# Kernel optimization log

Measured on AMD Instinct MI355X. Metric: run time of the kernel, lower is better.

Reference implementation:

```python
import jax, jax.numpy as jnp
import numpy as np

B, NPER, K = 32, 256, 32
N, E = B * NPER, B * NPER * 32
H, NF, NG, L = 128, 128, 50, 6
CUTOFF = 10.0
LOG2 = 0.6931471805599453


def _ssp(x):
    # ShiftedSoftplus: softplus(x) - log(2)
    return jax.nn.softplus(x) - LOG2


def setup_inputs() -> dict:
    key = jax.random.key(0)
    ks = jax.random.split(key, 16)
    rng = np.random.default_rng(0)

    pos = jnp.asarray(rng.uniform(0.0, 5.0, size=(N, 3)).astype(np.float32))
    z = jnp.asarray(rng.integers(1, 100, size=(N,)).astype(np.int32))
    batch = jnp.asarray((np.arange(N) // NPER).astype(np.int32))
    # K neighbors per atom, within the same graph, no self-loops; dst sorted
    dst = np.repeat(np.arange(N), K)
    off = rng.integers(1, NPER, size=N * K)
    src = (dst % NPER + off) % NPER + (dst // NPER) * NPER
    edge_index = jnp.asarray(np.stack([src, dst]).astype(np.int32))
    domain_ids = jnp.asarray(rng.integers(0, 5, size=(B,)).astype(np.int32))

    def dense(k, i, o):
        return jax.random.normal(k, (i, o), jnp.float32) / np.sqrt(i)

    def stackw(k, i, o):
        return jax.random.normal(k, (L, i, o), jnp.float32) / np.sqrt(i)

    return {
        'pos': pos, 'z': z, 'batch': batch, 'edge_index': edge_index,
        'domain_ids': domain_ids,
        'embedding': jax.random.normal(ks[0], (100, H), jnp.float32),
        'mlp_w1': stackw(ks[1], NG, NF), 'mlp_b1': jnp.zeros((L, NF), jnp.float32),
        'mlp_w2': stackw(ks[2], NF, NF), 'mlp_b2': jnp.zeros((L, NF), jnp.float32),
        'cf_lin1_w': stackw(ks[3], H, NF),
        'cf_lin2_w': stackw(ks[4], NF, H), 'cf_lin2_b': jnp.zeros((L, H), jnp.float32),
        'int_lin_w': stackw(ks[5], H, H), 'int_lin_b': jnp.zeros((L, H), jnp.float32),
        'out_w1': dense(ks[6], H, H // 2), 'out_b1': jnp.zeros((H // 2,), jnp.float32),
        'out_w2': dense(ks[7], H // 2, 1), 'out_b2': jnp.zeros((1,), jnp.float32),
        'dom_emb': jax.random.normal(ks[8], (5, 64), jnp.float32),
        'film_w1': dense(ks[9], 64, 128), 'film_b1': jnp.zeros((128,), jnp.float32),
        'film_w2': dense(ks[10], 128, 128), 'film_b2': jnp.zeros((128,), jnp.float32),
        'gamma_w': dense(ks[11], 128, H), 'gamma_b': jnp.zeros((H,), jnp.float32),
        'beta_w': dense(ks[12], 128, H), 'beta_b': jnp.zeros((H,), jnp.float32),
    }


def reference(pos, z, batch, edge_index, domain_ids, embedding,
              mlp_w1, mlp_b1, mlp_w2, mlp_b2, cf_lin1_w, cf_lin2_w, cf_lin2_b,
              int_lin_w, int_lin_b, out_w1, out_b1, out_w2, out_b2,
              dom_emb, film_w1, film_b1, film_w2, film_b2,
              gamma_w, gamma_b, beta_w, beta_b):
    n_atoms = pos.shape[0]
    n_graphs = domain_ids.shape[0]
    src, dst = edge_index[0], edge_index[1]

    # edge distances, gaussian smearing, cosine cutoff (computed once)
    d = jnp.sqrt(jnp.sum((pos[src] - pos[dst]) ** 2, axis=-1))          # [E]
    offsets = jnp.linspace(0.0, CUTOFF, NG).astype(pos.dtype)
    coeff = -0.5 / (CUTOFF / (NG - 1)) ** 2
    edge_attr = jnp.exp(coeff * (d[:, None] - offsets) ** 2)            # [E,NG]
    C = 0.5 * (jnp.cos(d * (np.pi / CUTOFF)) + 1.0)                     # [E]

    h = embedding[z]                                                    # [N,H]
    for l in range(L):
        # filter network on gaussian basis, modulated by cosine cutoff
        W = (_ssp(edge_attr @ mlp_w1[l] + mlp_b1[l]) @ mlp_w2[l] + mlp_b2[l]) * C[:, None]  # [E,NF]
        x = h @ cf_lin1_w[l]                                            # [N,NF]
        msg = x[src] * W                                                # [E,NF]
        agg = jax.ops.segment_sum(msg, dst, num_segments=n_atoms)       # [N,NF]
        x = agg @ cf_lin2_w[l] + cf_lin2_b[l]                           # [N,H]
        h = h + _ssp(x) @ int_lin_w[l] + int_lin_b[l]                   # residual

    atom_e = _ssp(h @ out_w1 + out_b1) @ out_w2 + out_b2                # [N,1]
    e_graph = jax.ops.segment_sum(atom_e, batch, num_segments=n_graphs) # [B,1]

    # FiLM domain bias (features are zeros, so gamma path contributes 0 - faithful)
    de = dom_emb[domain_ids]                                            # [B,64]
    film = jax.nn.relu(de @ film_w1 + film_b1) @ film_w2 + film_b2      # [B,128]
    gamma = film @ gamma_w + gamma_b                                    # [B,H]
    beta = film @ beta_w + beta_b                                       # [B,H]
    dummy = jnp.zeros((n_graphs, H), pos.dtype)
    bias = jnp.sum(gamma * dummy + beta, axis=-1)                       # [B]

    # faithful broadcast [B,1]+[B] -> [B,B], then sum(dim=1) as in original
    energy = jnp.sum(e_graph + bias[None, :], axis=1)                   # [B]

    forces = jnp.zeros((n_atoms, 3), energy.dtype)
    stress = jnp.zeros((n_graphs, 3, 3), energy.dtype)
    features = jnp.zeros((n_atoms, H), energy.dtype)
    return energy, forces, stress, features
```

## Files before the change

### kernel.cpp

```cpp
#include <hip/hip_runtime.h>
#include <math.h>

using uint = unsigned int;
typedef _Float16 h2    __attribute__((ext_vector_type(2)));
typedef _Float16 f16x8 __attribute__((ext_vector_type(8)));
typedef float    f32x4 __attribute__((ext_vector_type(4)));

#define N_ATOMS 8192
#define NEDGE   262144
#define KNBR    32
#define NGAUSS  50
#define NLAYER  6
#define NB      32
#define GTAB    1024
#define DMAX    8.6603f
#define FCUT    10.0f
#define MB      1048576

#define LSTRIDE 76
#define S_WT    0
#define S_AS    9728

#define WA_OFF  0
#define WB_OFF  8192
#define AS_OFF  16384
#define TS_OFF  17408
#define LAY_N   18432

#define T_W1    0
#define T_W2    4096
#define T_RBF   12288
#define T_HID   13312
#define TAB_SMEM 15360

#define OW1P_OFF 147456
#define M1_OFF   151552
#define M2_OFF   176128
#define WPACK_N  225280

__device__ __forceinline__ float ssp(float x) {
    return fmaxf(x, 0.0f) + log1pf(expf(-fabsf(x))) - 0.69314718055994531f;
}
__device__ __forceinline__ uint pack2(float a, float b) {
    union { h2 h; uint u; } x;
    h2 v; v.x = (_Float16)a; v.y = (_Float16)b; x.h = v; return x.u;
}
__device__ __forceinline__ h2 u2h(uint u) {
    union { uint u; h2 h; } x; x.u = u; return x.h;
}
__device__ __forceinline__ uint h2u(h2 h) {
    union { h2 h; uint u; } x; x.h = h; return x.u;
}
__device__ __forceinline__ float fdot2f(h2 a, h2 b, float c) {
#if __has_builtin(__builtin_amdgcn_fdot2)
    return __builtin_amdgcn_fdot2(a, b, c, false);
#else
    return fmaf((float)a.y, (float)b.y, fmaf((float)a.x, (float)b.x, c));
#endif
}

__device__ __forceinline__ int swz(int row, int quad) {
    return row * 64 + ((quad ^ (row & 15)) << 2);
}
__device__ __forceinline__ int swzc(int row, int c) {
    return row * 64 + (((c >> 2) ^ (row & 15)) << 2) + (c & 3);
}

__device__ __forceinline__ void stage_sw(uint* dst, const uint* __restrict__ src,
                                         int n16, int tid) {
    for (int i = tid; i < n16; i += 256) {
        uint4 v = ((const uint4*)src)[i];
        *(uint4*)&dst[swz(i >> 4, i & 15)] = v;
    }
}

template<int NCT>
__device__ __forceinline__ void run_gemm_sw(const uint* smA, const uint* smW,
                                            int lane, int nb, f32x4* acc) {
    int m = lane & 15, q = lane >> 4;
    #pragma unroll
    for (int ks = 0; ks < 4; ++ks) {
        int cq = q + ks * 4;
        f16x8 a = *(const f16x8*)&smA[swz(m, cq)];
        #pragma unroll
        for (int ct = 0; ct < NCT; ++ct) {
            int n = nb + ct * 16 + m;
            f16x8 b = *(const f16x8*)&smW[swz(n, cq)];
            acc[ct] = __builtin_amdgcn_mfma_f32_16x16x32_f16(a, b, acc[ct], 0, 0, 0);
        }
    }
}

template<int NCT>
__device__ __forceinline__ void run_gemm(const uint* sm, int as_off, int lane,
                                         int nb, f32x4* acc) {
    int m = lane & 15, q = lane >> 4;
    #pragma unroll
    for (int ks = 0; ks < 4; ++ks) {
        f16x8 a = *(const f16x8*)&sm[as_off + m * LSTRIDE + q * 4 + ks * 16];
        #pragma unroll
        for (int ct = 0; ct < NCT; ++ct) {
            f16x8 b = *(const f16x8*)&sm[S_WT + (nb + ct * 16 + m) * LSTRIDE + q * 4 + ks * 16];
            acc[ct] = __builtin_amdgcn_mfma_f32_16x16x32_f16(a, b, acc[ct], 0, 0, 0);
        }
    }
}

struct SArgs {
    const float *pos; const int *z; const int *ei; const int *dom;
    const float *emb;
    const float *cf1; const float *cf2w; const float *intw; const float *ow1;
    const float *mw1; const float *mw2;
    const float *dome; const float *fw1; const float *fb1;
    const float *fw2; const float *fb2; const float *bw; const float *bb;
    uint2 *epack; float *h; uint *xA;
    float *gbias; uint *wpack; float *out; int out_size;
};

__global__ void __launch_bounds__(256) k_setup(SArgs a) {
    __shared__ __align__(16) uint sm[S_AS + 1216];
    const int tid = threadIdx.x, bid = blockIdx.x;
    const int gidx = bid * 256 + tid, gsz = 512 * 256;
    const int lane = tid & 63, w = tid >> 6;
    const int m = lane & 15, q = lane >> 4;
    const int rowbase = bid * 16;

    for (int i = gidx; i < a.out_size; i += gsz) a.out[i] = 0.0f;

    for (int idx = gidx; idx < WPACK_N; idx += gsz) {
        if (idx < OW1P_OFF) {
            int mat = idx >> 13, e = idx & 8191;
            int kp = e >> 7, cc = e & 127;
            const float* src = (mat < 6) ? (a.cf1 + mat * 16384)
                            : (mat < 12) ? (a.cf2w + (mat - 6) * 16384)
                                         : (a.intw + (mat - 12) * 16384);
            a.wpack[mat * 8192 + cc * 64 + kp] =
                pack2(src[2 * kp * 128 + cc], src[(2 * kp + 1) * 128 + cc]);
        } else if (idx < M1_OFF) {
            int e = idx - OW1P_OFF;
            int kp = e >> 6, cc = e & 63;
            a.wpack[OW1P_OFF + cc * 64 + kp] =
                pack2(a.ow1[2 * kp * 64 + cc], a.ow1[(2 * kp + 1) * 64 + cc]);
        } else if (idx < M2_OFF) {
            int e = idx - M1_OFF;
            int l = e >> 12, r = e & 4095;
            int kp = r >> 7, cc = r & 127;
            int g0 = 2 * kp;
            float va = (g0 < NGAUSS)     ? a.mw1[l*NGAUSS*128 + g0*128 + cc]     : 0.f;
            float vb = (g0 + 1 < NGAUSS) ? a.mw1[l*NGAUSS*128 + (g0+1)*128 + cc] : 0.f;
            a.wpack[idx] = pack2(va, vb);
        } else {
            int e = idx - M2_OFF;
            int l = e >> 13, r = e & 8191;
            int kp = r >> 7, cc = r & 127;
            a.wpack[idx] = pack2(a.mw2[l*16384 + 2*kp*128 + cc],
                                 a.mw2[l*16384 + (2*kp+1)*128 + cc]);
        }
    }

    const float invdelta = (float)(GTAB - 1) / DMAX;
    #pragma unroll
    for (int t = 0; t < 2; ++t) {
        int e = rowbase * KNBR + t * 256 + tid;
        int s = a.ei[e], d = a.ei[NEDGE + e];
        float dx = a.pos[3*s] - a.pos[3*d];
        float dy = a.pos[3*s+1] - a.pos[3*d+1];
        float dz = a.pos[3*s+2] - a.pos[3*d+2];
        float dist = sqrtf(dx*dx + dy*dy + dz*dz);
        float u = dist * invdelta;
        int i0 = (int)u; i0 = (i0 < GTAB - 2) ? i0 : (GTAB - 2);
        float t2 = u - (float)i0;
        uint tb = pack2(t2, 0.0f) & 0xffffu;
        uint2 ep; ep.x = (uint)s; ep.y = (tb << 16) | (uint)i0;
        a.epack[e] = ep;
    }

    for (int i = tid; i < 1024; i += 256) {
        int r = i >> 6, f2 = i & 63;
        int zz = a.z[rowbase + r];
        float2 v = *(const float2*)&a.emb[zz * 128 + f2 * 2];
        *(float2*)&a.h[(rowbase + r) * 128 + f2 * 2] = v;
        sm[S_AS + r * LSTRIDE + f2] = pack2(v.x, v.y);
    }
    for (int i = tid; i < 2048; i += 256) {
        int m4 = i >> 7, cc = i & 127;
        float v[8];
        #pragma unroll
        for (int j = 0; j < 8; ++j) v[j] = a.cf1[(8 * m4 + j) * 128 + cc];
        uint4 pk; pk.x = pack2(v[0], v[1]); pk.y = pack2(v[2], v[3]);
        pk.z = pack2(v[4], v[5]); pk.w = pack2(v[6], v[7]);
        *(uint4*)&sm[cc * LSTRIDE + m4 * 4] = pk;
    }
    __syncthreads();
    {
        f32x4 acc[2] = {{0,0,0,0},{0,0,0,0}};
        run_gemm<2>(sm, S_AS, lane, w * 32, acc);
        #pragma unroll
        for (int ct = 0; ct < 2; ++ct) {
            int n = w * 32 + ct * 16 + m;
            #pragma unroll
            for (int i = 0; i < 4; ++i) {
                float v = acc[ct][i];
                float u = __shfl_xor(v, 1, 64);
                if (!(lane & 1))
                    a.xA[(rowbase + q * 4 + i) * 64 + (n >> 1)] = pack2(v, u);
            }
        }
    }
    __syncthreads();
    if (bid >= 32 && bid < 64) {
        int g = bid - 32;
        float* fs = (float*)sm;
        if (tid < 64) fs[tid] = a.dome[a.dom[g] * 64 + tid];
        __syncthreads();
        if (tid < 128) {
            float acc = a.fb1[tid];
            for (int i = 0; i < 64; ++i) acc = fmaf(fs[i], a.fw1[i*128 + tid], acc);
            fs[64 + tid] = fmaxf(acc, 0.0f);
        }
        __syncthreads();
        if (tid < 128) {
            float acc = a.fb2[tid];
            for (int i = 0; i < 128; ++i) acc = fmaf(fs[64+i], a.fw2[i*128 + tid], acc);
            fs[192 + tid] = acc;
        }
        __syncthreads();
        if (tid < 128) {
            float acc = a.bb[tid];
            for (int i = 0; i < 128; ++i) acc = fmaf(fs[192+i], a.bw[i*128 + tid], acc);
            #pragma unroll
            for (int off = 32; off > 0; off >>= 1) acc += __shfl_down(acc, off, 64);
            if ((tid & 63) == 0) fs[320 + (tid >> 6)] = acc;
        }
        __syncthreads();
        if (tid == 0) a.gbias[g] = fs[320] + fs[321];
    }
}

__global__ void __launch_bounds__(256) k_table(
    const uint* __restrict__ wpack, const float* __restrict__ mb1,
    const float* __restrict__ mb2, uint* __restrict__ tab2) {
    __shared__ __align__(16) uint sm[TAB_SMEM];
    const int tid = threadIdx.x;
    const int l = blockIdx.x >> 5;
    const int base = (blockIdx.x & 31) * 32;
    { const uint4* s4 = (const uint4*)(wpack + M1_OFF + l*4096);
      uint4* d4 = (uint4*)&sm[T_W1];
      for (int i = tid; i < 1024; i += 256) d4[i] = s4[i]; }
    { const uint4* s4 = (const uint4*)(wpack + M2_OFF + l*8192);
      uint4* d4 = (uint4*)&sm[T_W2];
      for (int i = tid; i < 2048; i += 256) d4[i] = s4[i]; }
    const float delta = DMAX / (float)(GTAB - 1);
    const float gstep = FCUT / (float)(NGAUSS - 1);
    const float coeff = -0.5f / (gstep * gstep);
    for (int i = tid; i < 1024; i += 256) {
        int r = i >> 5, kp = i & 31;
        float dv = (float)(base + r) * delta;
        int g0 = 2 * kp;
        float v0 = 0.f, v1 = 0.f;
        if (g0 < NGAUSS)     { float t = dv - (float)g0 * gstep;     v0 = expf(coeff*t*t); }
        if (g0 + 1 < NGAUSS) { float t = dv - (float)(g0+1) * gstep; v1 = expf(coeff*t*t); }
        sm[T_RBF + i] = pack2(v0, v1);
    }
    __syncthreads();
    int tx = tid & 31, ty = tid >> 5, c0 = tx * 4, tr0 = ty * 4;
    float acc[4][4];
    #pragma unroll
    for (int i = 0; i < 4; ++i) { acc[i][0]=0.f; acc[i][1]=0.f; acc[i][2]=0.f; acc[i][3]=0.f; }
    #pragma unroll
    for (int oct = 0; oct < 8; ++oct) {
        int kp0 = oct * 4;
        uint4 w_[4];
        #pragma unroll
        for (int p = 0; p < 4; ++p) w_[p] = *(const uint4*)&sm[T_W1 + (kp0+p)*128 + c0];
        #pragma unroll
        for (int i = 0; i < 4; ++i) {
            uint4 av = *(const uint4*)&sm[T_RBF + (tr0+i)*32 + kp0];
            uint aa[4] = {av.x, av.y, av.z, av.w};
            #pragma unroll
            for (int p = 0; p < 4; ++p) {
                h2 ap = u2h(aa[p]);
                acc[i][0] = fdot2f(ap, u2h(w_[p].x), acc[i][0]);
                acc[i][1] = fdot2f(ap, u2h(w_[p].y), acc[i][1]);
                acc[i][2] = fdot2f(ap, u2h(w_[p].z), acc[i][2]);
                acc[i][3] = fdot2f(ap, u2h(w_[p].w), acc[i][3]);
            }
        }
    }
    float4 b1v = *(const float4*)&mb1[l*128 + c0];
    #pragma unroll
    for (int i = 0; i < 4; ++i) {
        uint2 o;
        o.x = pack2(ssp(acc[i][0] + b1v.x), ssp(acc[i][1] + b1v.y));
        o.y = pack2(ssp(acc[i][2] + b1v.z), ssp(acc[i][3] + b1v.w));
        *(uint2*)&sm[T_HID + (tr0+i)*64 + (c0 >> 1)] = o;
    }
    __syncthreads();
    float acc2[4][4];
    #pragma unroll
    for (int i = 0; i < 4; ++i) { acc2[i][0]=0.f; acc2[i][1]=0.f; acc2[i][2]=0.f; acc2[i][3]=0.f; }
    #pragma unroll 4
    for (int oct = 0; oct < 16; ++oct) {
        int kp0 = oct * 4;
        uint4 w_[4];
        #pragma unroll
        for (int p = 0; p < 4; ++p) w_[p] = *(const uint4*)&sm[T_W2 + (kp0+p)*128 + c0];
        #pragma unroll
        for (int i = 0; i < 4; ++i) {
            uint4 av = *(const uint4*)&sm[T_HID + (tr0+i)*64 + kp0];
            uint aa[4] = {av.x, av.y, av.z, av.w};
            #pragma unroll
            for (int p = 0; p < 4; ++p) {
                h2 ap = u2h(aa[p]);
                acc2[i][0] = fdot2f(ap, u2h(w_[p].x), acc2[i][0]);
                acc2[i][1] = fdot2f(ap, u2h(w_[p].y), acc2[i][1]);
                acc2[i][2] = fdot2f(ap, u2h(w_[p].z), acc2[i][2]);
                acc2[i][3] = fdot2f(ap, u2h(w_[p].w), acc2[i][3]);
            }
        }
    }
    float4 b2v = *(const float4*)&mb2[l*128 + c0];
    #pragma unroll
    for (int i = 0; i < 4; ++i) {
        int row = base + tr0 + i;
        float dv = (float)row * delta;
        float Cd = 0.5f * (cosf(dv * 0.3141592653589793f) + 1.0f);
        uint2 o;
        o.x = pack2((acc2[i][0] + b2v.x)*Cd, (acc2[i][1] + b2v.y)*Cd);
        o.y = pack2((acc2[i][2] + b2v.z)*Cd, (acc2[i][3] + b2v.w)*Cd);
        *(uint2*)&tab2[(l*GTAB + row)*128 + tx*4] = o;
        if (row > 0)
            *(uint2*)&tab2[(l*GTAB + row - 1)*128 + tx*4 + 2] = o;
    }
}

template<bool LAST>
__global__ void __launch_bounds__(256) k_layer(
    float* __restrict__ h, const uint* __restrict__ xin, uint* __restrict__ xout,
    const uint* __restrict__ tab2l, const uint2* __restrict__ epack,
    const uint* __restrict__ w2p, const uint* __restrict__ w3p,
    const uint* __restrict__ w1np,
    const float* __restrict__ b2, const float* __restrict__ b3,
    const float* __restrict__ ob1, const float* __restrict__ ow2,
    const float* __restrict__ ob2, const float* __restrict__ gbias,
    float* __restrict__ out) {
    __shared__ __align__(16) uint sm[LAY_N];
    const int tid = threadIdx.x, bid = blockIdx.x;
    const int lane = tid & 63, w = tid >> 6;
    const int m = lane & 15, q = lane >> 4;
    const int xcd = bid & 7;
    const int j   = bid >> 3;
    const int g   = xcd * 4 + (j >> 4);
    const int sub = j & 15;
    const int rowbase = g * 256 + sub * 16;

    float hr[2][4];
    #pragma unroll
    for (int ct = 0; ct < 2; ++ct)
        #pragma unroll
        for (int i = 0; i < 4; ++i)
            hr[ct][i] = h[(rowbase + q * 4 + i) * 128 + w * 32 + ct * 16 + m];

    stage_sw(&sm[WA_OFF], w2p, 2048, tid);
    {
        const int side = lane >> 5, l5 = lane & 31;
        #pragma unroll
        for (int p = 0; p < 4; ++p) {
            int al = p * 4 + w;
            uint2 ep = epack[(rowbase + al) * KNBR + l5];
            h2 a0; a0.x = (_Float16)0; a0.y = (_Float16)0;
            h2 a1 = a0;
            #pragma unroll 4
            for (int k = 0; k < 16; ++k) {
                int e = 2 * k + side;
                uint s = __shfl(ep.x, e, 64);
                uint y = __shfl(ep.y, e, 64);
                int i0 = (int)(y & 0xffffu);
                uint th = y >> 16;
                h2 t2 = u2h(th | (th << 16));
                uint4 tv = *(const uint4*)&tab2l[i0 * 128 + l5 * 4];
                uint2 xv = *(const uint2*)&xin[s * 64 + l5 * 2];
                h2 w0 = u2h(tv.x) + t2 * (u2h(tv.z) - u2h(tv.x));
                h2 w1 = u2h(tv.y) + t2 * (u2h(tv.w) - u2h(tv.y));
                a0 = a0 + u2h(xv.x) * w0;
                a1 = a1 + u2h(xv.y) * w1;
            }
            uint u0 = h2u(a0), u1 = h2u(a1);
            uint p0 = __shfl_xor(u0, 32, 64), p1 = __shfl_xor(u1, 32, 64);
            if (side == 0) {
                h2 r0 = u2h(u0) + u2h(p0), r1 = u2h(u1) + u2h(p1);
                uint2 o; o.x = h2u(r0); o.y = h2u(r1);
                *(uint2*)&sm[AS_OFF + swzc(al, l5 * 2)] = o;
            }
        }
    }
    __syncthreads();
    stage_sw(&sm[WB_OFF], w3p, 2048, tid);
    {
        f32x4 acc[2] = {{0,0,0,0},{0,0,0,0}};
        run_gemm_sw<2>(&sm[AS_OFF], &sm[WA_OFF], lane, w * 32, acc);
        #pragma unroll
        for (int ct = 0; ct < 2; ++ct) {
            int n = w * 32 + ct * 16 + m;
            float bv = b2[n];
            #pragma unroll
            for (int i = 0; i < 4; ++i) {
                float v = ssp(acc[ct][i] + bv);
                float u = __shfl_xor(v, 1, 64);
                if (!(lane & 1))
                    sm[TS_OFF + swzc(q * 4 + i, n >> 1)] = pack2(v, u);
            }
        }
    }
    __syncthreads();
    stage_sw(&sm[WA_OFF], w1np, LAST ? 1024 : 2048, tid);
    {
        f32x4 acc[2] = {{0,0,0,0},{0,0,0,0}};
        run_gemm_sw<2>(&sm[TS_OFF], &sm[WB_OFF], lane, w * 32, acc);
        #pragma unroll
        for (int ct = 0; ct < 2; ++ct) {
            int n = w * 32 + ct * 16 + m;
            float bv = b3[n];
            #pragma unroll
            for (int i = 0; i < 4; ++i) {
                int r = rowbase + q * 4 + i;
                float hv = hr[ct][i] + acc[ct][i] + bv;
                h[r * 128 + n] = hv;
                float u = __shfl_xor(hv, 1, 64);
                if (!(lane & 1))
                    sm[AS_OFF + swzc(q * 4 + i, n >> 1)] = pack2(hv, u);
            }
        }
    }
    __syncthreads();
    if (!LAST) {
        f32x4 acc[2] = {{0,0,0,0},{0,0,0,0}};
        run_gemm_sw<2>(&sm[AS_OFF], &sm[WA_OFF], lane, w * 32, acc);
        #pragma unroll
        for (int ct = 0; ct < 2; ++ct) {
            int n = w * 32 + ct * 16 + m;
            #pragma unroll
            for (int i = 0; i < 4; ++i) {
                float v = acc[ct][i];
                float u = __shfl_xor(v, 1, 64);
                if (!(lane & 1))
                    xout[(rowbase + q * 4 + i) * 64 + (n >> 1)] = pack2(v, u);
            }
        }
    } else {
        f32x4 acc[1] = {{0,0,0,0}};
        run_gemm_sw<1>(&sm[AS_OFF], &sm[WA_OFF], lane, w * 16, acc);
        int n = w * 16 + m;
        float b1v = ob1[n], w2v = ow2[n];
        float part = 0.f;
        #pragma unroll
        for (int i = 0; i < 4; ++i) part += ssp(acc[0][i] + b1v) * w2v;
        #pragma unroll
        for (int mm = 1; mm < 64; mm <<= 1) part += __shfl_xor(part, mm, 64);
        float* fs = (float*)&sm[TS_OFF];
        if (lane == 0) fs[w] = part;
        __syncthreads();
        if (tid == 0) {
            float bsum = fs[0] + fs[1] + fs[2] + fs[3] + 16.0f * ob2[0];
            float add = 32.0f * bsum;
            if (sub == 0) {
                float sb = 0.f;
                for (int jj = 0; jj < NB; ++jj) sb += gbias[jj];
                add += sb;
            }
            atomicAdd(&out[g], add);
        }
    }
}

extern "C" void kernel_launch(void* const* d_in, const int* in_sizes, int n_in,
                              void* d_out, int out_size, void* d_ws, size_t ws_size,
                              hipStream_t stream) {
    SArgs a;
    a.pos  = (const float*)d_in[0];
    a.z    = (const int*)d_in[1];
    a.ei   = (const int*)d_in[3];
    a.dom  = (const int*)d_in[4];
    a.emb  = (const float*)d_in[5];
    a.mw1  = (const float*)d_in[6];
    const float* mb1 = (const float*)d_in[7];
    a.mw2  = (const float*)d_in[8];
    const float* mb2 = (const float*)d_in[9];
    a.cf1  = (const float*)d_in[10];
    a.cf2w = (const float*)d_in[11];
    const float* cf2b = (const float*)d_in[12];
    a.intw = (const float*)d_in[13];
    const float* intb = (const float*)d_in[14];
    a.ow1  = (const float*)d_in[15];
    const float* ob1  = (const float*)d_in[16];
    const float* ow2  = (const float*)d_in[17];
    const float* ob2  = (const float*)d_in[18];
    a.dome = (const float*)d_in[19];
    a.fw1  = (const float*)d_in[20];
    a.fb1  = (const float*)d_in[21];
    a.fw2  = (const float*)d_in[22];
    a.fb2  = (const float*)d_in[23];
    a.bw   = (const float*)d_in[26];
    a.bb   = (const float*)d_in[27];

    char* ws = (char*)d_ws;
    a.epack   = (uint2*)(ws + 0);
    uint* tab2= (uint*)(ws + 2*MB);
    a.h       = (float*)(ws + 5*MB);
    a.xA      = (uint*)(ws + 9*MB);
    uint* xB  = (uint*)(ws + 11*MB);
    a.gbias   = (float*)(ws + 15*MB);
    a.wpack   = (uint*)(ws + 15*MB + 4096);
    a.out = (float*)d_out;
    a.out_size = out_size;

    k_setup<<<512, 256, 0, stream>>>(a);
    k_table<<<192, 256, 0, stream>>>(a.wpack, mb1, mb2, tab2);

    const uint* xr = a.xA;
    uint* xw = xB;
    for (int l = 0; l < NLAYER; ++l) {
        const uint* w2p = a.wpack + (6 + l) * 8192;
        const uint* w3p = a.wpack + (12 + l) * 8192;
        if (l < NLAYER - 1) {
            k_layer<false><<<512, 256, 0, stream>>>(
                a.h, xr, xw, tab2 + l*GTAB*128, a.epack, w2p, w3p,
                a.wpack + (l + 1) * 8192,
                cf2b + l*128, intb + l*128, ob1, ow2, ob2, a.gbias, a.out);
        } else {
            k_layer<true><<<512, 256, 0, stream>>>(
                a.h, xr, xw, tab2 + l*GTAB*128, a.epack, w2p, w3p,
                a.wpack + OW1P_OFF,
                cf2b + l*128, intb + l*128, ob1, ow2, ob2, a.gbias, a.out);
        }
        const uint* tmp = xr; xr = xw; xw = (uint*)tmp;
    }
}
```

Baseline: 253.5 us.

## Fuse six layer launches into one persistent kernel with per-graph barriers

Merges the table-building kernel into the setup kernel by giving it extra blocks, and replaces the six per-layer launches with one fused kernel. That kernel loops over layers, keeps h in registers, and synchronizes the 16 blocks of each graph through an atomic counter barrier before moving to the next layer. This removes launch overhead and the h round-trip through global memory between layers. It relies on all 16 blocks of a graph being co-resident, and the spin-wait has a timeout that could silently break correctness. Each layer now writes to its own x buffer instead of ping-ponging between two.

```diff
diff --git a/kernel.cpp b/kernel.cpp
--- a/kernel.cpp
+++ b/kernel.cpp
@@ -17,6 +17,10 @@
 #define FCUT    10.0f
 #define MB      1048576
 
+#define NSETUP  512
+#define NTABLE  192
+#define NGRID   (NSETUP + NTABLE)
+
 #define LSTRIDE 76
 #define S_WT    0
 #define S_AS    9728
@@ -34,9 +38,8 @@
 #define TAB_SMEM 15360
 
 #define OW1P_OFF 147456
-#define M1_OFF   151552
-#define M2_OFF   176128
-#define WPACK_N  225280
+#define PACK_END 151552
+#define X_STR    524288
 
 __device__ __forceinline__ float ssp(float x) {
     return fmaxf(x, 0.0f) + log1pf(expf(-fabsf(x))) - 0.69314718055994531f;
@@ -110,24 +113,25 @@
     const float *pos; const int *z; const int *ei; const int *dom;
     const float *emb;
     const float *cf1; const float *cf2w; const float *intw; const float *ow1;
-    const float *mw1; const float *mw2;
+    const float *mw1; const float *mw2; const float *mb1; const float *mb2;
     const float *dome; const float *fw1; const float *fb1;
     const float *fw2; const float *fb2; const float *bw; const float *bb;
     uint2 *epack; float *h; uint *xA;
-    float *gbias; uint *wpack; float *out; int out_size;
+    float *gbias; uint *wpack; uint *tab2; uint *bar;
+    float *out; int out_size;
 };
 
 __global__ void __launch_bounds__(256) k_setup(SArgs a) {
-    __shared__ __align__(16) uint sm[S_AS + 1216];
+    __shared__ __align__(16) uint sm[TAB_SMEM];
     const int tid = threadIdx.x, bid = blockIdx.x;
-    const int gidx = bid * 256 + tid, gsz = 512 * 256;
+    const int gidx = bid * 256 + tid, gsz = NGRID * 256;
     const int lane = tid & 63, w = tid >> 6;
     const int m = lane & 15, q = lane >> 4;
-    const int rowbase = bid * 16;
 
     for (int i = gidx; i < a.out_size; i += gsz) a.out[i] = 0.0f;
-
-    for (int idx = gidx; idx < WPACK_N; idx += gsz) {
+    if (gidx < 256) a.bar[gidx] = 0u;
+
+    for (int idx = gidx; idx < PACK_END; idx += gsz) {
         if (idx < OW1P_OFF) {
             int mat = idx >> 13, e = idx & 8191;
             int kp = e >> 7, cc = e & 127;
@@ -136,214 +140,209 @@
                                          : (a.intw + (mat - 12) * 16384);
             a.wpack[mat * 8192 + cc * 64 + kp] =
                 pack2(src[2 * kp * 128 + cc], src[(2 * kp + 1) * 128 + cc]);
-        } else if (idx < M1_OFF) {
+        } else {
             int e = idx - OW1P_OFF;
             int kp = e >> 6, cc = e & 63;
             a.wpack[OW1P_OFF + cc * 64 + kp] =
                 pack2(a.ow1[2 * kp * 64 + cc], a.ow1[(2 * kp + 1) * 64 + cc]);
-        } else if (idx < M2_OFF) {
-            int e = idx - M1_OFF;
-            int l = e >> 12, r = e & 4095;
-            int kp = r >> 7, cc = r & 127;
-            int g0 = 2 * kp;
+        }
+    }
+
+    if (bid < NSETUP) {
+        const int rowbase = bid * 16;
+        const float invdelta = (float)(GTAB - 1) / DMAX;
+        #pragma unroll
+        for (int t = 0; t < 2; ++t) {
+            int e = rowbase * KNBR + t * 256 + tid;
+            int s = a.ei[e], d = a.ei[NEDGE + e];
+            float dx = a.pos[3*s] - a.pos[3*d];
+            float dy = a.pos[3*s+1] - a.pos[3*d+1];
+            float dz = a.pos[3*s+2] - a.pos[3*d+2];
+            float dist = sqrtf(dx*dx + dy*dy + dz*dz);
+            float u = dist * invdelta;
+            int i0 = (int)u; i0 = (i0 < GTAB - 2) ? i0 : (GTAB - 2);
+            float t2 = u - (float)i0;
+            uint tb = pack2(t2, 0.0f) & 0xffffu;
+            uint2 ep; ep.x = (uint)s; ep.y = (tb << 16) | (uint)i0;
+            a.epack[e] = ep;
+        }
+
+        for (int i = tid; i < 1024; i += 256) {
+            int r = i >> 6, f2 = i & 63;
+            int zz = a.z[rowbase + r];
+            float2 v = *(const float2*)&a.emb[zz * 128 + f2 * 2];
+            *(float2*)&a.h[(rowbase + r) * 128 + f2 * 2] = v;
+            sm[S_AS + r * LSTRIDE + f2] = pack2(v.x, v.y);
+        }
+        for (int i = tid; i < 2048; i += 256) {
+            int m4 = i >> 7, cc = i & 127;
+            float v[8];
+            #pragma unroll
+            for (int j = 0; j < 8; ++j) v[j] = a.cf1[(8 * m4 + j) * 128 + cc];
+            uint4 pk; pk.x = pack2(v[0], v[1]); pk.y = pack2(v[2], v[3]);
+            pk.z = pack2(v[4], v[5]); pk.w = pack2(v[6], v[7]);
+            *(uint4*)&sm[cc * LSTRIDE + m4 * 4] = pk;
+        }
+        __syncthreads();
+        {
+            f32x4 acc[2] = {{0,0,0,0},{0,0,0,0}};
+            run_gemm<2>(sm, S_AS, lane, w * 32, acc);
+            #pragma unroll
+            for (int ct = 0; ct < 2; ++ct) {
+                int n = w * 32 + ct * 16 + m;
+                #pragma unroll
+                for (int i = 0; i < 4; ++i) {
+                    float v = acc[ct][i];
+                    float u = __shfl_xor(v, 1, 64);
+                    if (!(lane & 1))
+                        a.xA[(rowbase + q * 4 + i) * 64 + (n >> 1)] = pack2(v, u);
+                }
+            }
+        }
+        __syncthreads();
+        if (bid >= 32 && bid < 64) {
+            int g = bid - 32;
+            float* fs = (float*)sm;
+            if (tid < 64) fs[tid] = a.dome[a.dom[g] * 64 + tid];
+            __syncthreads();
+            if (tid < 128) {
+                float acc = a.fb1[tid];
+                for (int i = 0; i < 64; ++i) acc = fmaf(fs[i], a.fw1[i*128 + tid], acc);
+                fs[64 + tid] = fmaxf(acc, 0.0f);
+            }
+            __syncthreads();
+            if (tid < 128) {
+                float acc = a.fb2[tid];
+                for (int i = 0; i < 128; ++i) acc = fmaf(fs[64+i], a.fw2[i*128 + tid], acc);
+                fs[192 + tid] = acc;
+            }
+            __syncthreads();
+            if (tid < 128) {
+                float acc = a.bb[tid];
+                for (int i = 0; i < 128; ++i) acc = fmaf(fs[192+i], a.bw[i*128 + tid], acc);
+                #pragma unroll
+                for (int off = 32; off > 0; off >>= 1) acc += __shfl_down(acc, off, 64);
+                if ((tid & 63) == 0) fs[320 + (tid >> 6)] = acc;
+            }
+            __syncthreads();
+            if (tid == 0) a.gbias[g] = fs[320] + fs[321];
+        }
+    } else {
+        const int tb = bid - NSETUP;
+        const int l = tb >> 5;
+        const int base = (tb & 31) * 32;
+        for (int i = tid; i < 4096; i += 256) {
+            int kp = i >> 7, cc = i & 127, g0 = 2 * kp;
             float va = (g0 < NGAUSS)     ? a.mw1[l*NGAUSS*128 + g0*128 + cc]     : 0.f;
             float vb = (g0 + 1 < NGAUSS) ? a.mw1[l*NGAUSS*128 + (g0+1)*128 + cc] : 0.f;
-            a.wpack[idx] = pack2(va, vb);
-        } else {
-            int e = idx - M2_OFF;
-            int l = e >> 13, r = e & 8191;
-            int kp = r >> 7, cc = r & 127;
-            a.wpack[idx] = pack2(a.mw2[l*16384 + 2*kp*128 + cc],
+            sm[T_W1 + i] = pack2(va, vb);
+        }
+        for (int i = tid; i < 8192; i += 256) {
+            int kp = i >> 7, cc = i & 127;
+            sm[T_W2 + i] = pack2(a.mw2[l*16384 + 2*kp*128 + cc],
                                  a.mw2[l*16384 + (2*kp+1)*128 + cc]);
         }
+        const float delta = DMAX / (float)(GTAB - 1);
+        const float gstep = FCUT / (float)(NGAUSS - 1);
+        const float coeff = -0.5f / (gstep * gstep);
+        for (int i = tid; i < 1024; i += 256) {
+            int r = i >> 5, kp = i & 31;
+            float dv = (float)(base + r) * delta;
+            int g0 = 2 * kp;
+            float v0 = 0.f, v1 = 0.f;
+            if (g0 < NGAUSS)     { float t = dv - (float)g0 * gstep;     v0 = expf(coeff*t*t); }
+            if (g0 + 1 < NGAUSS) { float t = dv - (float)(g0+1) * gstep; v1 = expf(coeff*t*t); }
+            sm[T_RBF + i] = pack2(v0, v1);
+        }
+        __syncthreads();
+        int tx = tid & 31, ty = tid >> 5, c0 = tx * 4, tr0 = ty * 4;
+        float acc[4][4];
+        #pragma unroll
+        for (int i = 0; i < 4; ++i) { acc[i][0]=0.f; acc[i][1]=0.f; acc[i][2]=0.f; acc[i][3]=0.f; }
+        #pragma unroll
+        for (int oct = 0; oct < 8; ++oct) {
+            int kp0 = oct * 4;
+            uint4 w_[4];
+            #pragma unroll
+            for (int p = 0; p < 4; ++p) w_[p] = *(const uint4*)&sm[T_W1 + (kp0+p)*128 + c0];
+            #pragma unroll
+            for (int i = 0; i < 4; ++i) {
+                uint4 av = *(const uint4*)&sm[T_RBF + (tr0+i)*32 + kp0];
+                uint aa[4] = {av.x, av.y, av.z, av.w};
+                #pragma unroll
+                for (int p = 0; p < 4; ++p) {
+                    h2 ap = u2h(aa[p]);
+                    acc[i][0] = fdot2f(ap, u2h(w_[p].x), acc[i][0]);
+                    acc[i][1] = fdot2f(ap, u2h(w_[p].y), acc[i][1]);
+                    acc[i][2] = fdot2f(ap, u2h(w_[p].z), acc[i][2]);
+                    acc[i][3] = fdot2f(ap, u2h(w_[p].w), acc[i][3]);
+                }
+            }
+        }
+        float4 b1v = *(const float4*)&a.mb1[l*128 + c0];
+        #pragma unroll
+        for (int i = 0; i < 4; ++i) {
+            uint2 o;
+            o.x = pack2(ssp(acc[i][0] + b1v.x), ssp(acc[i][1] + b1v.y));
+            o.y = pack2(ssp(acc[i][2] + b1v.z), ssp(acc[i][3] + b1v.w));
+            *(uint2*)&sm[T_HID + (tr0+i)*64 + (c0 >> 1)] = o;
+        }
+        __syncthreads();
+        float acc2[4][4];
+        #pragma unroll
+        for (int i = 0; i < 4; ++i) { acc2[i][0]=0.f; acc2[i][1]=0.f; acc2[i][2]=0.f; acc2[i][3]=0.f; }
+        #pragma unroll 4
+        for (int oct = 0; oct < 16; ++oct) {
+            int kp0 = oct * 4;
+            uint4 w_[4];
+            #pragma unroll
+            for (int p = 0; p < 4; ++p) w_[p] = *(const uint4*)&sm[T_W2 + (kp0+p)*128 + c0];
+            #pragma unroll
+            for (int i = 0; i < 4; ++i) {
+                uint4 av = *(const uint4*)&sm[T_HID + (tr0+i)*64 + kp0];
+                uint aa[4] = {av.x, av.y, av.z, av.w};
+                #pragma unroll
+                for (int p = 0; p < 4; ++p) {
+                    h2 ap = u2h(aa[p]);
+                    acc2[i][0] = fdot2f(ap, u2h(w_[p].x), acc2[i][0]);
+                    acc2[i][1] = fdot2f(ap, u2h(w_[p].y), acc2[i][1]);
+                    acc2[i][2] = fdot2f(ap, u2h(w_[p].z), acc2[i][2]);
+                    acc2[i][3] = fdot2f(ap, u2h(w_[p].w), acc2[i][3]);
+                }
+            }
+        }
+        float4 b2v = *(const float4*)&a.mb2[l*128 + c0];
+        #pragma unroll
+        for (int i = 0; i < 4; ++i) {
+            int row = base + tr0 + i;
+            float dv = (float)row * delta;
+            float Cd = 0.5f * (cosf(dv * 0.3141592653589793f) + 1.0f);
+            uint2 o;
+            o.x = pack2((acc2[i][0] + b2v.x)*Cd, (acc2[i][1] + b2v.y)*Cd);
+            o.y = pack2((acc2[i][2] + b2v.z)*Cd, (acc2[i][3] + b2v.w)*Cd);
+            *(uint2*)&a.tab2[(l*GTAB + row)*128 + tx*4] = o;
+            if (row > 0)
+                *(uint2*)&a.tab2[(l*GTAB + row - 1)*128 + tx*4 + 2] = o;
+        }
     }
-
-    const float invdelta = (float)(GTAB - 1) / DMAX;
-    #pragma unroll
-    for (int t = 0; t < 2; ++t) {
-        int e = rowbase * KNBR + t * 256 + tid;
-        int s = a.ei[e], d = a.ei[NEDGE + e];
-        float dx = a.pos[3*s] - a.pos[3*d];
-        float dy = a.pos[3*s+1] - a.pos[3*d+1];
-        float dz = a.pos[3*s+2] - a.pos[3*d+2];
-        float dist = sqrtf(dx*dx + dy*dy + dz*dz);
-        float u = dist * invdelta;
-        int i0 = (int)u; i0 = (i0 < GTAB - 2) ? i0 : (GTAB - 2);
-        float t2 = u - (float)i0;
-        uint tb = pack2(t2, 0.0f) & 0xffffu;
-        uint2 ep; ep.x = (uint)s; ep.y = (tb << 16) | (uint)i0;
-        a.epack[e] = ep;
-    }
-
-    for (int i = tid; i < 1024; i += 256) {
-        int r = i >> 6, f2 = i & 63;
-        int zz = a.z[rowbase + r];
-        float2 v = *(const float2*)&a.emb[zz * 128 + f2 * 2];
-        *(float2*)&a.h[(rowbase + r) * 128 + f2 * 2] = v;
-        sm[S_AS + r * LSTRIDE + f2] = pack2(v.x, v.y);
-    }
-    for (int i = tid; i < 2048; i += 256) {
-        int m4 = i >> 7, cc = i & 127;
-        float v[8];
-        #pragma unroll
-        for (int j = 0; j < 8; ++j) v[j] = a.cf1[(8 * m4 + j) * 128 + cc];
-        uint4 pk; pk.x = pack2(v[0], v[1]); pk.y = pack2(v[2], v[3]);
-        pk.z = pack2(v[4], v[5]); pk.w = pack2(v[6], v[7]);
-        *(uint4*)&sm[cc * LSTRIDE + m4 * 4] = pk;
-    }
-    __syncthreads();
-    {
-        f32x4 acc[2] = {{0,0,0,0},{0,0,0,0}};
-        run_gemm<2>(sm, S_AS, lane, w * 32, acc);
-        #pragma unroll
-        for (int ct = 0; ct < 2; ++ct) {
-            int n = w * 32 + ct * 16 + m;
-            #pragma unroll
-            for (int i = 0; i < 4; ++i) {
-                float v = acc[ct][i];
-                float u = __shfl_xor(v, 1, 64);
-                if (!(lane & 1))
-                    a.xA[(rowbase + q * 4 + i) * 64 + (n >> 1)] = pack2(v, u);
-            }
-        }
-    }
-    __syncthreads();
-    if (bid >= 32 && bid < 64) {
-        int g = bid - 32;
-        float* fs = (float*)sm;
-        if (tid < 64) fs[tid] = a.dome[a.dom[g] * 64 + tid];
-        __syncthreads();
-        if (tid < 128) {
-            float acc = a.fb1[tid];
-            for (int i = 0; i < 64; ++i) acc = fmaf(fs[i], a.fw1[i*128 + tid], acc);
-            fs[64 + tid] = fmaxf(acc, 0.0f);
-        }
-        __syncthreads();
-        if (tid < 128) {
-            float acc = a.fb2[tid];
-            for (int i = 0; i < 128; ++i) acc = fmaf(fs[64+i], a.fw2[i*128 + tid], acc);
-            fs[192 + tid] = acc;
-        }
-        __syncthreads();
-        if (tid < 128) {
-            float acc = a.bb[tid];
-            for (int i = 0; i < 128; ++i) acc = fmaf(fs[192+i], a.bw[i*128 + tid], acc);
-            #pragma unroll
-            for (int off = 32; off > 0; off >>= 1) acc += __shfl_down(acc, off, 64);
-            if ((tid & 63) == 0) fs[320 + (tid >> 6)] = acc;
-        }
-        __syncthreads();
-        if (tid == 0) a.gbias[g] = fs[320] + fs[321];
-    }
-}
-
-__global__ void __launch_bounds__(256) k_table(
-    const uint* __restrict__ wpack, const float* __restrict__ mb1,
-    const float* __restrict__ mb2, uint* __restrict__ tab2) {
-    __shared__ __align__(16) uint sm[TAB_SMEM];
-    const int tid = threadIdx.x;
-    const int l = blockIdx.x >> 5;
-    const int base = (blockIdx.x & 31) * 32;
-    { const uint4* s4 = (const uint4*)(wpack + M1_OFF + l*4096);
-      uint4* d4 = (uint4*)&sm[T_W1];
-      for (int i = tid; i < 1024; i += 256) d4[i] = s4[i]; }
-    { const uint4* s4 = (const uint4*)(wpack + M2_OFF + l*8192);
-      uint4* d4 = (uint4*)&sm[T_W2];
-      for (int i = tid; i < 2048; i += 256) d4[i] = s4[i]; }
-    const float delta = DMAX / (float)(GTAB - 1);
-    const float gstep = FCUT / (float)(NGAUSS - 1);
-    const float coeff = -0.5f / (gstep * gstep);
-    for (int i = tid; i < 1024; i += 256) {
-        int r = i >> 5, kp = i & 31;
-        float dv = (float)(base + r) * delta;
-        int g0 = 2 * kp;
-        float v0 = 0.f, v1 = 0.f;
-        if (g0 < NGAUSS)     { float t = dv - (float)g0 * gstep;     v0 = expf(coeff*t*t); }
-        if (g0 + 1 < NGAUSS) { float t = dv - (float)(g0+1) * gstep; v1 = expf(coeff*t*t); }
-        sm[T_RBF + i] = pack2(v0, v1);
-    }
-    __syncthreads();
-    int tx = tid & 31, ty = tid >> 5, c0 = tx * 4, tr0 = ty * 4;
-    float acc[4][4];
-    #pragma unroll
-    for (int i = 0; i < 4; ++i) { acc[i][0]=0.f; acc[i][1]=0.f; acc[i][2]=0.f; acc[i][3]=0.f; }
-    #pragma unroll
-    for (int oct = 0; oct < 8; ++oct) {
-        int kp0 = oct * 4;
-        uint4 w_[4];
-        #pragma unroll
-        for (int p = 0; p < 4; ++p) w_[p] = *(const uint4*)&sm[T_W1 + (kp0+p)*128 + c0];
-        #pragma unroll
-        for (int i = 0; i < 4; ++i) {
-            uint4 av = *(const uint4*)&sm[T_RBF + (tr0+i)*32 + kp0];
-            uint aa[4] = {av.x, av.y, av.z, av.w};
-            #pragma unroll
-            for (int p = 0; p < 4; ++p) {
-                h2 ap = u2h(aa[p]);
-                acc[i][0] = fdot2f(ap, u2h(w_[p].x), acc[i][0]);
-                acc[i][1] = fdot2f(ap, u2h(w_[p].y), acc[i][1]);
-                acc[i][2] = fdot2f(ap, u2h(w_[p].z), acc[i][2]);
-                acc[i][3] = fdot2f(ap, u2h(w_[p].w), acc[i][3]);
-            }
-        }
-    }
-    float4 b1v = *(const float4*)&mb1[l*128 + c0];
-    #pragma unroll
-    for (int i = 0; i < 4; ++i) {
-        uint2 o;
-        o.x = pack2(ssp(acc[i][0] + b1v.x), ssp(acc[i][1] + b1v.y));
-        o.y = pack2(ssp(acc[i][2] + b1v.z), ssp(acc[i][3] + b1v.w));
-        *(uint2*)&sm[T_HID + (tr0+i)*64 + (c0 >> 1)] = o;
-    }
-    __syncthreads();
-    float acc2[4][4];
-    #pragma unroll
-    for (int i = 0; i < 4; ++i) { acc2[i][0]=0.f; acc2[i][1]=0.f; acc2[i][2]=0.f; acc2[i][3]=0.f; }
-    #pragma unroll 4
-    for (int oct = 0; oct < 16; ++oct) {
-        int kp0 = oct * 4;
-        uint4 w_[4];
-        #pragma unroll
-        for (int p = 0; p < 4; ++p) w_[p] = *(const uint4*)&sm[T_W2 + (kp0+p)*128 + c0];
-        #pragma unroll
-        for (int i = 0; i < 4; ++i) {
-            uint4 av = *(const uint4*)&sm[T_HID + (tr0+i)*64 + kp0];
-            uint aa[4] = {av.x, av.y, av.z, av.w};
-            #pragma unroll
-            for (int p = 0; p < 4; ++p) {
-                h2 ap = u2h(aa[p]);
-                acc2[i][0] = fdot2f(ap, u2h(w_[p].x), acc2[i][0]);
-                acc2[i][1] = fdot2f(ap, u2h(w_[p].y), acc2[i][1]);
-                acc2[i][2] = fdot2f(ap, u2h(w_[p].z), acc2[i][2]);
-                acc2[i][3] = fdot2f(ap, u2h(w_[p].w), acc2[i][3]);
-            }
-        }
-    }
-    float4 b2v = *(const float4*)&mb2[l*128 + c0];
-    #pragma unroll
-    for (int i = 0; i < 4; ++i) {
-        int row = base + tr0 + i;
-        float dv = (float)row * delta;
-        float Cd = 0.5f * (cosf(dv * 0.3141592653589793f) + 1.0f);
-        uint2 o;
-        o.x = pack2((acc2[i][0] + b2v.x)*Cd, (acc2[i][1] + b2v.y)*Cd);
-        o.y = pack2((acc2[i][2] + b2v.z)*Cd, (acc2[i][3] + b2v.w)*Cd);
-        *(uint2*)&tab2[(l*GTAB + row)*128 + tx*4] = o;
-        if (row > 0)
-            *(uint2*)&tab2[(l*GTAB + row - 1)*128 + tx*4 + 2] = o;
-    }
-}
-
-template<bool LAST>
-__global__ void __launch_bounds__(256) k_layer(
-    float* __restrict__ h, const uint* __restrict__ xin, uint* __restrict__ xout,
-    const uint* __restrict__ tab2l, const uint2* __restrict__ epack,
-    const uint* __restrict__ w2p, const uint* __restrict__ w3p,
-    const uint* __restrict__ w1np,
-    const float* __restrict__ b2, const float* __restrict__ b3,
-    const float* __restrict__ ob1, const float* __restrict__ ow2,
-    const float* __restrict__ ob2, const float* __restrict__ gbias,
-    float* __restrict__ out) {
+}
+
+struct LArgs {
+    const float* h;
+    const uint* x0;
+    uint* xb;
+    const uint* tab2;
+    const uint2* epack;
+    const uint* wpack;
+    const float* cf2b;
+    const float* intb;
+    const float* ob1; const float* ow2; const float* ob2;
+    const float* gbias;
+    float* out;
+    uint* bar;
+};
+
+__global__ void __launch_bounds__(256, 2) k_fused(LArgs a) {
     __shared__ __align__(16) uint sm[LAY_N];
     const int tid = threadIdx.x, bid = blockIdx.x;
     const int lane = tid & 63, w = tid >> 6;
@@ -359,116 +358,141 @@
     for (int ct = 0; ct < 2; ++ct)
         #pragma unroll
         for (int i = 0; i < 4; ++i)
-            hr[ct][i] = h[(rowbase + q * 4 + i) * 128 + w * 32 + ct * 16 + m];
-
-    stage_sw(&sm[WA_OFF], w2p, 2048, tid);
-    {
-        const int side = lane >> 5, l5 = lane & 31;
-        #pragma unroll
-        for (int p = 0; p < 4; ++p) {
-            int al = p * 4 + w;
-            uint2 ep = epack[(rowbase + al) * KNBR + l5];
-            h2 a0; a0.x = (_Float16)0; a0.y = (_Float16)0;
-            h2 a1 = a0;
-            #pragma unroll 4
-            for (int k = 0; k < 16; ++k) {
-                int e = 2 * k + side;
-                uint s = __shfl(ep.x, e, 64);
-                uint y = __shfl(ep.y, e, 64);
-                int i0 = (int)(y & 0xffffu);
-                uint th = y >> 16;
-                h2 t2 = u2h(th | (th << 16));
-                uint4 tv = *(const uint4*)&tab2l[i0 * 128 + l5 * 4];
-                uint2 xv = *(const uint2*)&xin[s * 64 + l5 * 2];
-                h2 w0 = u2h(tv.x) + t2 * (u2h(tv.z) - u2h(tv.x));
-                h2 w1 = u2h(tv.y) + t2 * (u2h(tv.w) - u2h(tv.y));
-                a0 = a0 + u2h(xv.x) * w0;
-                a1 = a1 + u2h(xv.y) * w1;
-            }
-            uint u0 = h2u(a0), u1 = h2u(a1);
-            uint p0 = __shfl_xor(u0, 32, 64), p1 = __shfl_xor(u1, 32, 64);
-            if (side == 0) {
-                h2 r0 = u2h(u0) + u2h(p0), r1 = u2h(u1) + u2h(p1);
-                uint2 o; o.x = h2u(r0); o.y = h2u(r1);
-                *(uint2*)&sm[AS_OFF + swzc(al, l5 * 2)] = o;
-            }
-        }
-    }
-    __syncthreads();
-    stage_sw(&sm[WB_OFF], w3p, 2048, tid);
-    {
-        f32x4 acc[2] = {{0,0,0,0},{0,0,0,0}};
-        run_gemm_sw<2>(&sm[AS_OFF], &sm[WA_OFF], lane, w * 32, acc);
-        #pragma unroll
-        for (int ct = 0; ct < 2; ++ct) {
-            int n = w * 32 + ct * 16 + m;
-            float bv = b2[n];
-            #pragma unroll
-            for (int i = 0; i < 4; ++i) {
-                float v = ssp(acc[ct][i] + bv);
-                float u = __shfl_xor(v, 1, 64);
-                if (!(lane & 1))
-                    sm[TS_OFF + swzc(q * 4 + i, n >> 1)] = pack2(v, u);
-            }
-        }
-    }
-    __syncthreads();
-    stage_sw(&sm[WA_OFF], w1np, LAST ? 1024 : 2048, tid);
-    {
-        f32x4 acc[2] = {{0,0,0,0},{0,0,0,0}};
-        run_gemm_sw<2>(&sm[TS_OFF], &sm[WB_OFF], lane, w * 32, acc);
-        #pragma unroll
-        for (int ct = 0; ct < 2; ++ct) {
-            int n = w * 32 + ct * 16 + m;
-            float bv = b3[n];
-            #pragma unroll
-            for (int i = 0; i < 4; ++i) {
-                int r = rowbase + q * 4 + i;
-                float hv = hr[ct][i] + acc[ct][i] + bv;
-                h[r * 128 + n] = hv;
-                float u = __shfl_xor(hv, 1, 64);
-                if (!(lane & 1))
-                    sm[AS_OFF + swzc(q * 4 + i, n >> 1)] = pack2(hv, u);
-            }
-        }
-    }
-    __syncthreads();
-    if (!LAST) {
-        f32x4 acc[2] = {{0,0,0,0},{0,0,0,0}};
-        run_gemm_sw<2>(&sm[AS_OFF], &sm[WA_OFF], lane, w * 32, acc);
-        #pragma unroll
-        for (int ct = 0; ct < 2; ++ct) {
-            int n = w * 32 + ct * 16 + m;
-            #pragma unroll
-            for (int i = 0; i < 4; ++i) {
-                float v = acc[ct][i];
-                float u = __shfl_xor(v, 1, 64);
-                if (!(lane & 1))
-                    xout[(rowbase + q * 4 + i) * 64 + (n >> 1)] = pack2(v, u);
-            }
-        }
-    } else {
-        f32x4 acc[1] = {{0,0,0,0}};
-        run_gemm_sw<1>(&sm[AS_OFF], &sm[WA_OFF], lane, w * 16, acc);
-        int n = w * 16 + m;
-        float b1v = ob1[n], w2v = ow2[n];
-        float part = 0.f;
-        #pragma unroll
-        for (int i = 0; i < 4; ++i) part += ssp(acc[0][i] + b1v) * w2v;
-        #pragma unroll
-        for (int mm = 1; mm < 64; mm <<= 1) part += __shfl_xor(part, mm, 64);
-        float* fs = (float*)&sm[TS_OFF];
-        if (lane == 0) fs[w] = part;
-        __syncthreads();
-        if (tid == 0) {
-            float bsum = fs[0] + fs[1] + fs[2] + fs[3] + 16.0f * ob2[0];
-            float add = 32.0f * bsum;
-            if (sub == 0) {
-                float sb = 0.f;
-                for (int jj = 0; jj < NB; ++jj) sb += gbias[jj];
-                add += sb;
-            }
-            atomicAdd(&out[g], add);
+            hr[ct][i] = a.h[(rowbase + q * 4 + i) * 128 + w * 32 + ct * 16 + m];
+
+    const uint* xr = a.x0;
+    uint* xw = a.xb;
+
+    #pragma unroll 1
+    for (int l = 0; l < NLAYER; ++l) {
+        const bool last = (l == NLAYER - 1);
+        const uint* w2p  = a.wpack + (6 + l) * 8192;
+        const uint* w3p  = a.wpack + (12 + l) * 8192;
+        const uint* w1np = last ? (a.wpack + OW1P_OFF) : (a.wpack + (l + 1) * 8192);
+        const uint* tabl = a.tab2 + l * (GTAB * 128);
+        const float* b2 = a.cf2b + l * 128;
+        const float* b3 = a.intb + l * 128;
+
+        stage_sw(&sm[WA_OFF], w2p, 2048, tid);
+        {
+            const int side = lane >> 5, l5 = lane & 31;
+            #pragma unroll
+            for (int p = 0; p < 4; ++p) {
+                int al = p * 4 + w;
+                uint2 ep = a.epack[(rowbase + al) * KNBR + l5];
+                h2 a0; a0.x = (_Float16)0; a0.y = (_Float16)0;
+                h2 a1 = a0;
+                #pragma unroll 4
+                for (int k = 0; k < 16; ++k) {
+                    int e = 2 * k + side;
+                    uint s = __shfl(ep.x, e, 64);
+                    uint y = __shfl(ep.y, e, 64);
+                    int i0 = (int)(y & 0xffffu);
+                    uint th = y >> 16;
+                    h2 t2 = u2h(th | (th << 16));
+                    uint4 tv = *(const uint4*)&tabl[i0 * 128 + l5 * 4];
+                    uint2 xv = *(const uint2*)&xr[(int)s * 64 + l5 * 2];
+                    h2 w0 = u2h(tv.x) + t2 * (u2h(tv.z) - u2h(tv.x));
+                    h2 w1 = u2h(tv.y) + t2 * (u2h(tv.w) - u2h(tv.y));
+                    a0 = a0 + u2h(xv.x) * w0;
+                    a1 = a1 + u2h(xv.y) * w1;
+                }
+                uint u0 = h2u(a0), u1 = h2u(a1);
+                uint p0 = __shfl_xor(u0, 32, 64), p1 = __shfl_xor(u1, 32, 64);
+                if (side == 0) {
+                    h2 r0 = u2h(u0) + u2h(p0), r1 = u2h(u1) + u2h(p1);
+                    uint2 o; o.x = h2u(r0); o.y = h2u(r1);
+                    *(uint2*)&sm[AS_OFF + swzc(al, l5 * 2)] = o;
+                }
+            }
+        }
+        __syncthreads();
+        stage_sw(&sm[WB_OFF], w3p, 2048, tid);
+        {
+            f32x4 acc[2] = {{0,0,0,0},{0,0,0,0}};
+            run_gemm_sw<2>(&sm[AS_OFF], &sm[WA_OFF], lane, w * 32, acc);
+            #pragma unroll
+            for (int ct = 0; ct < 2; ++ct) {
+                int n = w * 32 + ct * 16 + m;
+                float bv = b2[n];
+                #pragma unroll
+                for (int i = 0; i < 4; ++i) {
+                    float v = ssp(acc[ct][i] + bv);
+                    float u = __shfl_xor(v, 1, 64);
+                    if (!(lane & 1))
+                        sm[TS_OFF + swzc(q * 4 + i, n >> 1)] = pack2(v, u);
+                }
+            }
+        }
+        __syncthreads();
+        stage_sw(&sm[WA_OFF], w1np, last ? 1024 : 2048, tid);
+        {
+            f32x4 acc[2] = {{0,0,0,0},{0,0,0,0}};
+            run_gemm_sw<2>(&sm[TS_OFF], &sm[WB_OFF], lane, w * 32, acc);
+            #pragma unroll
+            for (int ct = 0; ct < 2; ++ct) {
+                int n = w * 32 + ct * 16 + m;
+                float bv = b3[n];
+                #pragma unroll
+                for (int i = 0; i < 4; ++i) {
+                    float hv = hr[ct][i] + acc[ct][i] + bv;
+                    hr[ct][i] = hv;
+                    float u = __shfl_xor(hv, 1, 64);
+                    if (!(lane & 1))
+                        sm[AS_OFF + swzc(q * 4 + i, n >> 1)] = pack2(hv, u);
+                }
+            }
+        }
+        __syncthreads();
+        if (!last) {
+            f32x4 acc[2] = {{0,0,0,0},{0,0,0,0}};
+            run_gemm_sw<2>(&sm[AS_OFF], &sm[WA_OFF], lane, w * 32, acc);
+            #pragma unroll
+            for (int ct = 0; ct < 2; ++ct) {
+                int n = w * 32 + ct * 16 + m;
+                #pragma unroll
+                for (int i = 0; i < 4; ++i) {
+                    float v = acc[ct][i];
+                    float u = __shfl_xor(v, 1, 64);
+                    if (!(lane & 1))
+                        xw[(rowbase + q * 4 + i) * 64 + (n >> 1)] = pack2(v, u);
+                }
+            }
+            __syncthreads();
+            if (tid == 0) {
+                uint* c = a.bar + l * NB + g;
+                __hip_atomic_fetch_add(c, 1u, __ATOMIC_RELEASE, __HIP_MEMORY_SCOPE_AGENT);
+                int it = 0;
+                while (__hip_atomic_load(c, __ATOMIC_RELAXED, __HIP_MEMORY_SCOPE_AGENT) < 16u
+                       && ++it < (1 << 18))
+                    __builtin_amdgcn_s_sleep(1);
+                __builtin_amdgcn_fence(__ATOMIC_ACQUIRE, "agent");
+            }
+            __syncthreads();
+            xr = xw; xw += X_STR;
+        } else {
+            f32x4 acc[1] = {{0,0,0,0}};
+            run_gemm_sw<1>(&sm[AS_OFF], &sm[WA_OFF], lane, w * 16, acc);
+            int n = w * 16 + m;
+            float b1v = a.ob1[n], w2v = a.ow2[n];
+            float part = 0.f;
+            #pragma unroll
+            for (int i = 0; i < 4; ++i) part += ssp(acc[0][i] + b1v) * w2v;
+            #pragma unroll
+            for (int mm = 1; mm < 64; mm <<= 1) part += __shfl_xor(part, mm, 64);
+            float* fs = (float*)&sm[TS_OFF];
+            if (lane == 0) fs[w] = part;
+            __syncthreads();
+            if (tid == 0) {
+                float bsum = fs[0] + fs[1] + fs[2] + fs[3] + 16.0f * a.ob2[0];
+                float add = 32.0f * bsum;
+                if (sub == 0) {
+                    float sb = 0.f;
+                    for (int jj = 0; jj < NB; ++jj) sb += a.gbias[jj];
+                    add += sb;
+                }
+                atomicAdd(&a.out[g], add);
+            }
         }
     }
 }
@@ -483,9 +507,9 @@
     a.dom  = (const int*)d_in[4];
     a.emb  = (const float*)d_in[5];
     a.mw1  = (const float*)d_in[6];
-    const float* mb1 = (const float*)d_in[7];
+    a.mb1  = (const float*)d_in[7];
     a.mw2  = (const float*)d_in[8];
-    const float* mb2 = (const float*)d_in[9];
+    a.mb2  = (const float*)d_in[9];
     a.cf1  = (const float*)d_in[10];
     a.cf2w = (const float*)d_in[11];
     const float* cf2b = (const float*)d_in[12];
@@ -505,34 +529,24 @@
 
     char* ws = (char*)d_ws;
     a.epack   = (uint2*)(ws + 0);
-    uint* tab2= (uint*)(ws + 2*MB);
+    a.tab2    = (uint*)(ws + 2*MB);
     a.h       = (float*)(ws + 5*MB);
     a.xA      = (uint*)(ws + 9*MB);
-    uint* xB  = (uint*)(ws + 11*MB);
-    a.gbias   = (float*)(ws + 15*MB);
-    a.wpack   = (uint*)(ws + 15*MB + 4096);
+    uint* xb  = (uint*)(ws + 11*MB);
+    a.gbias   = (float*)(ws + 21*MB);
+    a.bar     = (uint*)(ws + 21*MB + 4096);
+    a.wpack   = (uint*)(ws + 21*MB + 8192);
     a.out = (float*)d_out;
     a.out_size = out_size;
 
-    k_setup<<<512, 256, 0, stream>>>(a);
-    k_table<<<192, 256, 0, stream>>>(a.wpack, mb1, mb2, tab2);
-
-    const uint* xr = a.xA;
-    uint* xw = xB;
-    for (int l = 0; l < NLAYER; ++l) {
-        const uint* w2p = a.wpack + (6 + l) * 8192;
-        const uint* w3p = a.wpack + (12 + l) * 8192;
-        if (l < NLAYER - 1) {
-            k_layer<false><<<512, 256, 0, stream>>>(
-                a.h, xr, xw, tab2 + l*GTAB*128, a.epack, w2p, w3p,
-                a.wpack + (l + 1) * 8192,
-                cf2b + l*128, intb + l*128, ob1, ow2, ob2, a.gbias, a.out);
-        } else {
-            k_layer<true><<<512, 256, 0, stream>>>(
-                a.h, xr, xw, tab2 + l*GTAB*128, a.epack, w2p, w3p,
-                a.wpack + OW1P_OFF,
-                cf2b + l*128, intb + l*128, ob1, ow2, ob2, a.gbias, a.out);
-        }
-        const uint* tmp = xr; xr = xw; xw = (uint*)tmp;
-    }
-}
+    k_setup<<<NGRID, 256, 0, stream>>>(a);
+
+    LArgs la;
+    la.h = a.h; la.x0 = a.xA; la.xb = xb;
+    la.tab2 = a.tab2; la.epack = a.epack; la.wpack = a.wpack;
+    la.cf2b = cf2b; la.intb = intb;
+    la.ob1 = ob1; la.ow2 = ow2; la.ob2 = ob2;
+    la.gbias = a.gbias; la.out = (float*)d_out; la.bar = a.bar;
+
+    k_fused<<<dim3(512), dim3(256), 0, stream>>>(la);
+}
```

New measurement: 365.4 us. +44.1%, slower.
